# Optimization experiments

Hardware: AMD Instinct MI355X
Metric: run time of the kernel (lower is better)

Reference implementation:

```python
import jax, jax.numpy as jnp
import numpy as np

N, D = 16384, 512
LOGIT_SCALE = 14.285714  # 1/0.07, standard CLIP temperature


def setup_inputs() -> dict:
    key = jax.random.key(0)
    k1, k2 = jax.random.split(key)
    image_features = jax.random.normal(k1, (N, D), dtype=jnp.float32)
    text_features = jax.random.normal(k2, (N, D), dtype=jnp.float32)
    logit_scale = jnp.asarray(LOGIT_SCALE, dtype=jnp.float32)
    return {
        "image_features": image_features,
        "text_features": text_features,
        "logit_scale": logit_scale,
    }


def reference(image_features, text_features, logit_scale):
    # logits_per_image = scale * img @ txt.T  -> [N, N]
    # logits_per_text is its transpose, so compute the GEMM once.
    logits = logit_scale * jnp.einsum("nd,md->nm", image_features, text_features)
    diag = jnp.diagonal(logits)  # correct-pair logits (labels = arange)
    # cross_entropy with label i on row i: logsumexp(row) - logit[i,i]
    loss_i = jnp.mean(jax.nn.logsumexp(logits, axis=1) - diag)
    # text loss uses transposed logits -> column-wise logsumexp
    loss_t = jnp.mean(jax.nn.logsumexp(logits, axis=0) - diag)
    return (loss_i + loss_t) * 0.5
```

## Files before the change

### kernel.cpp

```cpp
#include <hip/hip_runtime.h>
#include <hip/hip_bf16.h>

#define N_ 16384
#define D_ 512
#define BM 256
#define BN 256
#define BK 64
#define NT (D_ / BK)
#define NBLK (N_ / BM)
#define BUFB 32768

typedef __attribute__((ext_vector_type(8))) __bf16 bf16x8;
typedef __attribute__((ext_vector_type(4))) float f32x4;

#define GLDS(gptr, lptr)                                                              \
  __builtin_amdgcn_global_load_lds((const __attribute__((address_space(1))) void*)(gptr), \
                                   (__attribute__((address_space(3))) void*)(lptr), 16, 0, 0)

__device__ inline unsigned short f2bf(float f) {
  __hip_bfloat16 h = __float2bfloat16(f);
  return *reinterpret_cast<unsigned short*>(&h);
}

__global__ void cvt_bf16_kernel(const float* __restrict__ src,
                                unsigned short* __restrict__ dst, long n,
                                const float* __restrict__ scale_p) {
  const float s = scale_p ? scale_p[0] : 1.0f;
  long i = ((long)blockIdx.x * blockDim.x + threadIdx.x) * 8;
  const long stride = (long)gridDim.x * blockDim.x * 8;
  typedef __attribute__((ext_vector_type(8))) unsigned short us8;
  for (; i < n; i += stride) {
    const float4* sp = (const float4*)(src + i);
    float4 f0 = sp[0], f1 = sp[1];
    us8 v;
    v[0] = f2bf(f0.x * s); v[1] = f2bf(f0.y * s); v[2] = f2bf(f0.z * s); v[3] = f2bf(f0.w * s);
    v[4] = f2bf(f1.x * s); v[5] = f2bf(f1.y * s); v[6] = f2bf(f1.z * s); v[7] = f2bf(f1.w * s);
    *(us8*)(dst + i) = v;
  }
}

__global__ __launch_bounds__(512, 2)
void gemm_lse_kernel(const unsigned short* __restrict__ A,
                     const unsigned short* __restrict__ B,
                     float2* __restrict__ rowMS,
                     float2* __restrict__ colMS,
                     float* __restrict__ diag) {
  __shared__ __align__(16) unsigned short As[2][BM][BK];
  __shared__ __align__(16) unsigned short Bs[2][BN][BK];

  const int t = threadIdx.x;
  const int l = t & 63;
  const int wid = t >> 6;
  const int wr = wid >> 2;
  const int wc = wid & 3;

  int id = blockIdx.x;
  id = (id & 7) * (NBLK * NBLK / 8) + (id >> 3);
  const int br = id / NBLK;
  const int bc = id % NBLK;

  const int srow = t >> 3;
  const int scol = (((t & 7) ^ (srow & 7)) << 3);

  const unsigned short* aBase = A + (size_t)(br * BM + srow) * D_ + scol;
  const unsigned short* bBase = B + (size_t)(bc * BN + srow) * D_ + scol;

  f32x4 acc[8][4];
#pragma unroll
  for (int m = 0; m < 8; ++m)
#pragma unroll
    for (int n = 0; n < 4; ++n) acc[m][n] = (f32x4)0.0f;

  const int swz = (l & 7) << 4;
  const char* asb = (const char*)As;
  const char* bsb = (const char*)Bs;

#define STAGE(kt_, b_)                                              \
  {                                                                 \
    const unsigned short* ag_ = aBase + (kt_)*BK;                   \
    const unsigned short* bg_ = bBase + (kt_)*BK;                   \
    char* al_ = (char*)As + (b_)*BUFB + t * 16;                     \
    char* bl_ = (char*)Bs + (b_)*BUFB + t * 16;                     \
    _Pragma("unroll") for (int c_ = 0; c_ < 4; ++c_) {              \
      GLDS(ag_ + c_ * 64 * D_, al_ + c_ * 8192);                    \
      GLDS(bg_ + c_ * 64 * D_, bl_ + c_ * 8192);                    \
    }                                                               \
  }

  STAGE(0, 0);
  STAGE(1, 1);

#pragma unroll
  for (int kt = 0; kt < NT; ++kt) {
    const int b = kt & 1;
    if (kt == NT - 1) { asm volatile("s_waitcnt vmcnt(0)" ::: "memory"); }
    else              { asm volatile("s_waitcnt vmcnt(8)" ::: "memory"); }
    __builtin_amdgcn_sched_barrier(0);
    __builtin_amdgcn_s_barrier();
    __builtin_amdgcn_sched_barrier(0);

#pragma unroll
    for (int kk = 0; kk < 2; ++kk) {
      const int cbk = kk * 64 + (l >> 4) * 16;
      bf16x8 af[8], bfv[4];
#pragma unroll
      for (int m = 0; m < 8; ++m)
        af[m] = *(const bf16x8*)(asb + b * BUFB +
                                 (wr * 128 + m * 16 + (l & 15)) * 128 + (cbk ^ swz));
#pragma unroll
      for (int n = 0; n < 4; ++n)
        bfv[n] = *(const bf16x8*)(bsb + b * BUFB +
                                  (wc * 64 + n * 16 + (l & 15)) * 128 + (cbk ^ swz));
      __builtin_amdgcn_s_setprio(1);
#pragma unroll
      for (int m = 0; m < 8; ++m)
#pragma unroll
        for (int n = 0; n < 4; ++n)
          acc[m][n] = __builtin_amdgcn_mfma_f32_16x16x32_bf16(af[m], bfv[n], acc[m][n], 0, 0, 0);
      __builtin_amdgcn_s_setprio(0);
    }

    asm volatile("s_waitcnt lgkmcnt(0)" ::: "memory");
    __builtin_amdgcn_sched_barrier(0);
    __builtin_amdgcn_s_barrier();
    __builtin_amdgcn_sched_barrier(0);
    if (kt + 2 < NT) STAGE(kt + 2, b);
  }
#undef STAGE

  float* rowb = (float*)As;
  float* colb = rowb + 4 * 256 * 2;

  if (br == bc) {
#pragma unroll
    for (int m = 0; m < 8; ++m)
#pragma unroll
      for (int n = 0; n < 4; ++n)
#pragma unroll
        for (int r = 0; r < 4; ++r) {
          const int row = wr * 128 + m * 16 + (l >> 4) * 4 + r;
          const int col = wc * 64 + n * 16 + (l & 15);
          if (row == col) diag[br * BM + row] = acc[m][n][r];
        }
  }

#pragma unroll
  for (int m = 0; m < 8; ++m) {
#pragma unroll
    for (int r = 0; r < 4; ++r) {
      float mx = fmaxf(fmaxf(acc[m][0][r], acc[m][1][r]), fmaxf(acc[m][2][r], acc[m][3][r]));
#pragma unroll
      for (int off = 1; off < 16; off <<= 1) mx = fmaxf(mx, __shfl_xor(mx, off, 64));
      float s = 0.f;
#pragma unroll
      for (int n = 0; n < 4; ++n) s += __expf(acc[m][n][r] - mx);
#pragma unroll
      for (int off = 1; off < 16; off <<= 1) s += __shfl_xor(s, off, 64);
      if ((l & 15) == 0) {
        const int row = wr * 128 + m * 16 + (l >> 4) * 4 + r;
        rowb[(wc * 256 + row) * 2 + 0] = mx;
        rowb[(wc * 256 + row) * 2 + 1] = s;
      }
    }
  }

#pragma unroll
  for (int n = 0; n < 4; ++n) {
    float mx = -1e30f;
#pragma unroll
    for (int m = 0; m < 8; ++m)
#pragma unroll
      for (int r = 0; r < 4; ++r) mx = fmaxf(mx, acc[m][n][r]);
    mx = fmaxf(mx, __shfl_xor(mx, 16, 64));
    mx = fmaxf(mx, __shfl_xor(mx, 32, 64));
    float s = 0.f;
#pragma unroll
    for (int m = 0; m < 8; ++m)
#pragma unroll
      for (int r = 0; r < 4; ++r) s += __expf(acc[m][n][r] - mx);
    s += __shfl_xor(s, 16, 64);
    s += __shfl_xor(s, 32, 64);
    if ((l >> 4) == 0) {
      const int col = wc * 64 + n * 16 + l;
      colb[(wr * 256 + col) * 2 + 0] = mx;
      colb[(wr * 256 + col) * 2 + 1] = s;
    }
  }
  __syncthreads();

  if (t < 256) {
    float mm = -1e30f, ss = 0.f;
#pragma unroll
    for (int w = 0; w < 4; ++w) {
      float m0 = rowb[(w * 256 + t) * 2 + 0], s0 = rowb[(w * 256 + t) * 2 + 1];
      float nm = fmaxf(mm, m0);
      ss = ss * __expf(mm - nm) + s0 * __expf(m0 - nm);
      mm = nm;
    }
    rowMS[(size_t)bc * N_ + br * BM + t] = make_float2(mm, ss);
  } else {
    const int c = t - 256;
    float mm = -1e30f, ss = 0.f;
#pragma unroll
    for (int w = 0; w < 2; ++w) {
      float m0 = colb[(w * 256 + c) * 2 + 0], s0 = colb[(w * 256 + c) * 2 + 1];
      float nm = fmaxf(mm, m0);
      ss = ss * __expf(mm - nm) + s0 * __expf(m0 - nm);
      mm = nm;
    }
    colMS[(size_t)br * N_ + bc * BN + c] = make_float2(mm, ss);
  }
}

__global__ void reduce1_kernel(const float2* __restrict__ rowMS,
                               const float2* __restrict__ colMS,
                               const float* __restrict__ diag,
                               float* __restrict__ partials) {
  const int tid = blockIdx.x * blockDim.x + threadIdx.x;
  float m = -1e30f, s = 0.f;
  if (tid < N_) {
    const int r = tid;
    for (int cb = 0; cb < NBLK; ++cb) {
      float2 p = rowMS[(size_t)cb * N_ + r];
      float nm = fmaxf(m, p.x);
      s = s * __expf(m - nm) + p.y * __expf(p.x - nm);
      m = nm;
    }
    m = m + logf(s) - diag[r];
  } else {
    const int c = tid - N_;
    for (int rb = 0; rb < NBLK; ++rb) {
      float2 p = colMS[(size_t)rb * N_ + c];
      float nm = fmaxf(m, p.x);
      s = s * __expf(m - nm) + p.y * __expf(p.x - nm);
      m = nm;
    }
    m = m + logf(s) - diag[c];
  }
  float val = m;
#pragma unroll
  for (int off = 1; off < 64; off <<= 1) val += __shfl_xor(val, off, 64);
  __shared__ float red[4];
  if ((threadIdx.x & 63) == 0) red[threadIdx.x >> 6] = val;
  __syncthreads();
  if (threadIdx.x == 0) partials[blockIdx.x] = red[0] + red[1] + red[2] + red[3];
}

__global__ void reduce2_kernel(const float* __restrict__ partials, float* __restrict__ out) {
  const int t = threadIdx.x;
  float v = partials[t] + partials[t + 64];
#pragma unroll
  for (int off = 1; off < 64; off <<= 1) v += __shfl_xor(v, off, 64);
  if (t == 0) out[0] = v * (1.0f / (2.0f * (float)N_));
}

extern "C" void kernel_launch(void* const* d_in, const int* in_sizes, int n_in,
                              void* d_out, int out_size, void* d_ws, size_t ws_size,
                              hipStream_t stream) {
  const float* img = (const float*)d_in[0];
  const float* txt = (const float*)d_in[1];
  const float* scale = (const float*)d_in[2];
  float* out = (float*)d_out;

  char* ws = (char*)d_ws;
  size_t off = 0;
  unsigned short* imgB = (unsigned short*)(ws + off); off += (size_t)N_ * D_ * 2;
  unsigned short* txtB = (unsigned short*)(ws + off); off += (size_t)N_ * D_ * 2;
  float2* rowMS = (float2*)(ws + off); off += (size_t)NBLK * N_ * sizeof(float2);
  float2* colMS = (float2*)(ws + off); off += (size_t)NBLK * N_ * sizeof(float2);
  float* diag = (float*)(ws + off); off += (size_t)N_ * sizeof(float);
  float* partials = (float*)(ws + off); off += 128 * sizeof(float);
  (void)ws_size; (void)in_sizes; (void)n_in; (void)out_size;

  cvt_bf16_kernel<<<1024, 256, 0, stream>>>(img, imgB, (long)N_ * D_, scale);
  cvt_bf16_kernel<<<1024, 256, 0, stream>>>(txt, txtB, (long)N_ * D_, nullptr);
  gemm_lse_kernel<<<NBLK * NBLK, 512, 0, stream>>>(imgB, txtB, rowMS, colMS, diag);
  reduce1_kernel<<<(2 * N_) / 256, 256, 0, stream>>>(rowMS, colMS, diag, partials);
  reduce2_kernel<<<1, 64, 0, stream>>>(partials, out);
}
```

Measured before the change: 468.7 us.

## Restructure GEMM main loop into fine-grained phases interleaving LDS loads, prefetch and MFMA

Splits each K tile into two 32-wide halves stored as separate LDS regions with a new rotation-based swizzle. The loop becomes four phases per tile, each loading fragments, issuing part of the next global-to-LDS prefetch, then running a block of MFMAs between barriers. This is meant to overlap global loads, LDS reads and matrix math more evenly and to reduce bank conflicts. It adds more barriers per tile and tighter vmcnt bookkeeping, which could introduce stalls or races if the wait counts are off.

Measured after the change: 511.9 us. +9.2%, slower.

```diff
diff --git a/kernel.cpp b/kernel.cpp
--- a/kernel.cpp
+++ b/kernel.cpp
@@ -8,7 +8,7 @@
 #define BK 64
 #define NT (D_ / BK)
 #define NBLK (N_ / BM)
-#define BUFB 32768
+#define REGB 16384
 
 typedef __attribute__((ext_vector_type(8))) __bf16 bf16x8;
 typedef __attribute__((ext_vector_type(4))) float f32x4;
@@ -16,6 +16,8 @@
 #define GLDS(gptr, lptr)                                                              \
   __builtin_amdgcn_global_load_lds((const __attribute__((address_space(1))) void*)(gptr), \
                                    (__attribute__((address_space(3))) void*)(lptr), 16, 0, 0)
+
+#define MFMA(a, b, c) __builtin_amdgcn_mfma_f32_16x16x32_bf16((a), (b), (c), 0, 0, 0)
 
 __device__ inline unsigned short f2bf(float f) {
   __hip_bfloat16 h = __float2bfloat16(f);
@@ -45,8 +47,8 @@
                      float2* __restrict__ rowMS,
                      float2* __restrict__ colMS,
                      float* __restrict__ diag) {
-  __shared__ __align__(16) unsigned short As[2][BM][BK];
-  __shared__ __align__(16) unsigned short Bs[2][BN][BK];
+  __shared__ __align__(16) unsigned short As[2][2][256][32];
+  __shared__ __align__(16) unsigned short Bs[2][2][256][32];
 
   const int t = threadIdx.x;
   const int l = t & 63;
@@ -59,11 +61,23 @@
   const int br = id / NBLK;
   const int bc = id % NBLK;
 
-  const int srow = t >> 3;
-  const int scol = (((t & 7) ^ (srow & 7)) << 3);
-
-  const unsigned short* aBase = A + (size_t)(br * BM + srow) * D_ + scol;
-  const unsigned short* bBase = B + (size_t)(bc * BN + srow) * D_ + scol;
+  const int sr0 = t >> 2;
+  const int sc0 = ((t & 3) - (t >> 3)) & 3;
+
+  const unsigned short* aSt = A + (size_t)(br * BM + sr0) * D_ + sc0 * 8;
+  const unsigned short* bSt = B + (size_t)(bc * BN + sr0) * D_ + sc0 * 8;
+
+  int offA[8], offB[4];
+#pragma unroll
+  for (int m = 0; m < 8; ++m) {
+    const int row = wr * 128 + m * 16 + (l & 15);
+    offA[m] = row * 64 + ((((l >> 4) + (row >> 1)) & 3) << 4);
+  }
+#pragma unroll
+  for (int n = 0; n < 4; ++n) {
+    const int row = wc * 64 + n * 16 + (l & 15);
+    offB[n] = row * 64 + ((((l >> 4) + (row >> 1)) & 3) << 4);
+  }
 
   f32x4 acc[8][4];
 #pragma unroll
@@ -71,62 +85,99 @@
 #pragma unroll
     for (int n = 0; n < 4; ++n) acc[m][n] = (f32x4)0.0f;
 
-  const int swz = (l & 7) << 4;
   const char* asb = (const char*)As;
   const char* bsb = (const char*)Bs;
-
-#define STAGE(kt_, b_)                                              \
-  {                                                                 \
-    const unsigned short* ag_ = aBase + (kt_)*BK;                   \
-    const unsigned short* bg_ = bBase + (kt_)*BK;                   \
-    char* al_ = (char*)As + (b_)*BUFB + t * 16;                     \
-    char* bl_ = (char*)Bs + (b_)*BUFB + t * 16;                     \
-    _Pragma("unroll") for (int c_ = 0; c_ < 4; ++c_) {              \
-      GLDS(ag_ + c_ * 64 * D_, al_ + c_ * 8192);                    \
-      GLDS(bg_ + c_ * 64 * D_, bl_ + c_ * 8192);                    \
-    }                                                               \
-  }
-
-  STAGE(0, 0);
-  STAGE(1, 1);
-
-#pragma unroll
-  for (int kt = 0; kt < NT; ++kt) {
-    const int b = kt & 1;
-    if (kt == NT - 1) { asm volatile("s_waitcnt vmcnt(0)" ::: "memory"); }
-    else              { asm volatile("s_waitcnt vmcnt(8)" ::: "memory"); }
-    __builtin_amdgcn_sched_barrier(0);
-    __builtin_amdgcn_s_barrier();
-    __builtin_amdgcn_sched_barrier(0);
-
-#pragma unroll
-    for (int kk = 0; kk < 2; ++kk) {
-      const int cbk = kk * 64 + (l >> 4) * 16;
-      bf16x8 af[8], bfv[4];
-#pragma unroll
-      for (int m = 0; m < 8; ++m)
-        af[m] = *(const bf16x8*)(asb + b * BUFB +
-                                 (wr * 128 + m * 16 + (l & 15)) * 128 + (cbk ^ swz));
-#pragma unroll
-      for (int n = 0; n < 4; ++n)
-        bfv[n] = *(const bf16x8*)(bsb + b * BUFB +
-                                  (wc * 64 + n * 16 + (l & 15)) * 128 + (cbk ^ swz));
-      __builtin_amdgcn_s_setprio(1);
-#pragma unroll
-      for (int m = 0; m < 8; ++m)
-#pragma unroll
-        for (int n = 0; n < 4; ++n)
-          acc[m][n] = __builtin_amdgcn_mfma_f32_16x16x32_bf16(af[m], bfv[n], acc[m][n], 0, 0, 0);
-      __builtin_amdgcn_s_setprio(0);
-    }
-
-    asm volatile("s_waitcnt lgkmcnt(0)" ::: "memory");
-    __builtin_amdgcn_sched_barrier(0);
-    __builtin_amdgcn_s_barrier();
-    __builtin_amdgcn_sched_barrier(0);
-    if (kt + 2 < NT) STAGE(kt + 2, b);
-  }
-#undef STAGE
+  bf16x8 af[8], bfv[4];
+
+#define STG(gbase, lds, S_, K_, kt_)                                   \
+  {                                                                    \
+    const unsigned short* g_ = (gbase) + (kt_)*BK + (K_)*32;           \
+    char* d_ = (char*)(lds) + ((S_)*2 + (K_)) * REGB + t * 16;         \
+    GLDS(g_, d_);                                                      \
+    GLDS(g_ + 128 * D_, d_ + 8192);                                    \
+  }
+
+  STG(aSt, As, 0, 0, 0); STG(bSt, Bs, 0, 0, 0);
+  STG(aSt, As, 0, 1, 0); STG(bSt, Bs, 0, 1, 0);
+  STG(aSt, As, 1, 0, 1); STG(bSt, Bs, 1, 0, 1);
+  STG(aSt, As, 1, 1, 1);
+  asm volatile("s_waitcnt vmcnt(6)" ::: "memory");
+  __builtin_amdgcn_sched_barrier(0);
+  __builtin_amdgcn_s_barrier();
+
+#define PH_SYNC()                                          \
+  __builtin_amdgcn_s_barrier();                            \
+  asm volatile("s_waitcnt lgkmcnt(0)" ::: "memory");       \
+  __builtin_amdgcn_sched_barrier(0);                       \
+  __builtin_amdgcn_s_setprio(1);
+
+#define PH_END()                                           \
+  __builtin_amdgcn_s_setprio(0);                           \
+  __builtin_amdgcn_s_barrier();
+
+#define TILE(T_, S_)                                                          \
+  {                                                                           \
+                                                   \
+    _Pragma("unroll") for (int m = 0; m < 8; ++m)                             \
+        af[m] = *(const bf16x8*)(asb + ((S_)*2 + 0) * REGB + offA[m]);        \
+    bfv[0] = *(const bf16x8*)(bsb + ((S_)*2 + 0) * REGB + offB[0]);           \
+    bfv[1] = *(const bf16x8*)(bsb + ((S_)*2 + 0) * REGB + offB[1]);           \
+    if ((T_) + 1 < NT) STG(bSt, Bs, ((S_) ^ 1), 1, (T_) + 1);                 \
+    if ((T_) == NT - 1) {                                                     \
+      asm volatile("s_waitcnt vmcnt(0)" ::: "memory");                        \
+      __builtin_amdgcn_sched_barrier(0);                                      \
+    }                                                                         \
+    PH_SYNC();                                                                \
+    _Pragma("unroll") for (int m = 0; m < 8; ++m) {                           \
+      acc[m][0] = MFMA(af[m], bfv[0], acc[m][0]);                             \
+      acc[m][1] = MFMA(af[m], bfv[1], acc[m][1]);                             \
+    }                                                                         \
+    PH_END();                                                                 \
+                                                   \
+    bfv[2] = *(const bf16x8*)(bsb + ((S_)*2 + 0) * REGB + offB[2]);           \
+    bfv[3] = *(const bf16x8*)(bsb + ((S_)*2 + 0) * REGB + offB[3]);           \
+    if ((T_) + 2 < NT) STG(aSt, As, (S_), 0, (T_) + 2);                       \
+    PH_SYNC();                                                                \
+    _Pragma("unroll") for (int m = 0; m < 8; ++m) {                           \
+      acc[m][2] = MFMA(af[m], bfv[2], acc[m][2]);                             \
+      acc[m][3] = MFMA(af[m], bfv[3], acc[m][3]);                             \
+    }                                                                         \
+    PH_END();                                                                 \
+                                                   \
+    _Pragma("unroll") for (int m = 0; m < 8; ++m)                             \
+        af[m] = *(const bf16x8*)(asb + ((S_)*2 + 1) * REGB + offA[m]);        \
+    bfv[0] = *(const bf16x8*)(bsb + ((S_)*2 + 1) * REGB + offB[0]);           \
+    bfv[1] = *(const bf16x8*)(bsb + ((S_)*2 + 1) * REGB + offB[1]);           \
+    if ((T_) + 2 < NT) STG(bSt, Bs, (S_), 0, (T_) + 2);                       \
+    PH_SYNC();                                                                \
+    _Pragma("unroll") for (int m = 0; m < 8; ++m) {                           \
+      acc[m][0] = MFMA(af[m], bfv[0], acc[m][0]);                             \
+      acc[m][1] = MFMA(af[m], bfv[1], acc[m][1]);                             \
+    }                                                                         \
+    PH_END();                                                                 \
+                                                   \
+    bfv[2] = *(const bf16x8*)(bsb + ((S_)*2 + 1) * REGB + offB[2]);           \
+    bfv[3] = *(const bf16x8*)(bsb + ((S_)*2 + 1) * REGB + offB[3]);           \
+    if ((T_) + 2 < NT) STG(aSt, As, (S_), 1, (T_) + 2);                       \
+    asm volatile("s_waitcnt vmcnt(6)" ::: "memory");                          \
+    __builtin_amdgcn_sched_barrier(0);                                        \
+    PH_SYNC();                                                                \
+    _Pragma("unroll") for (int m = 0; m < 8; ++m) {                           \
+      acc[m][2] = MFMA(af[m], bfv[2], acc[m][2]);                             \
+      acc[m][3] = MFMA(af[m], bfv[3], acc[m][3]);                             \
+    }                                                                         \
+    PH_END();                                                                 \
+  }
+
+#pragma unroll 1
+  for (int tp = 0; tp < NT; tp += 2) {
+    TILE(tp, 0);
+    TILE(tp + 1, 1);
+  }
+#undef TILE
+#undef PH_SYNC
+#undef PH_END
+#undef STG
 
   float* rowb = (float*)As;
   float* colb = rowb + 4 * 256 * 2;
```

## Triple-buffer BK=32 LDS pipeline with split A/B staging and exp2-domain softmax

Applied to the files above, without the earlier changes.

Reworks the GEMM main loop from a double-buffered BK=64 scheme to a three-slot BK=32 ring. Each k-step is split into two half-M MFMA phases, with A and B prefetches interleaved between them and finer vmcnt waits, so loads overlap compute more closely. It also changes the block-index swizzle and the LDS swizzle pattern, and keeps separate LDS arrays for the epilogue reductions. Separately, log2(e) is folded into the bf16 conversion scale so the epilogue can use exp2f and log2f, with ln2 applied back at the end. The extra barriers per k-step and the smaller K tile could add synchronization overhead.

Measured after the change: 501.1 us. 1.07x slower.

```diff
diff --git a/kernel.cpp b/kernel.cpp
--- a/kernel.cpp
+++ b/kernel.cpp
@@ -5,10 +5,10 @@
 #define D_ 512
 #define BM 256
 #define BN 256
-#define BK 64
+#define BK 32
 #define NT (D_ / BK)
 #define NBLK (N_ / BM)
-#define BUFB 32768
+#define SLOTB 16384
 
 typedef __attribute__((ext_vector_type(8))) __bf16 bf16x8;
 typedef __attribute__((ext_vector_type(4))) float f32x4;
@@ -17,6 +17,8 @@
   __builtin_amdgcn_global_load_lds((const __attribute__((address_space(1))) void*)(gptr), \
                                    (__attribute__((address_space(3))) void*)(lptr), 16, 0, 0)
 
+#define MFMA16(a, b, c) __builtin_amdgcn_mfma_f32_16x16x32_bf16((a), (b), (c), 0, 0, 0)
+
 __device__ inline unsigned short f2bf(float f) {
   __hip_bfloat16 h = __float2bfloat16(f);
   return *reinterpret_cast<unsigned short*>(&h);
@@ -25,7 +27,7 @@
 __global__ void cvt_bf16_kernel(const float* __restrict__ src,
                                 unsigned short* __restrict__ dst, long n,
                                 const float* __restrict__ scale_p) {
-  const float s = scale_p ? scale_p[0] : 1.0f;
+  const float s = scale_p ? scale_p[0] * 1.4426950408889634f : 1.0f;
   long i = ((long)blockIdx.x * blockDim.x + threadIdx.x) * 8;
   const long stride = (long)gridDim.x * blockDim.x * 8;
   typedef __attribute__((ext_vector_type(8))) unsigned short us8;
@@ -45,8 +47,10 @@
                      float2* __restrict__ rowMS,
                      float2* __restrict__ colMS,
                      float* __restrict__ diag) {
-  __shared__ __align__(16) unsigned short As[2][BM][BK];
-  __shared__ __align__(16) unsigned short Bs[2][BN][BK];
+  __shared__ __align__(16) unsigned short AL[3][2][128][32];
+  __shared__ __align__(16) unsigned short BL[3][2][128][32];
+  __shared__ float rowb[4][256][2];
+  __shared__ float colb[2][256][2];
 
   const int t = threadIdx.x;
   const int l = t & 63;
@@ -54,16 +58,32 @@
   const int wr = wid >> 2;
   const int wc = wid & 3;
 
-  int id = blockIdx.x;
-  id = (id & 7) * (NBLK * NBLK / 8) + (id >> 3);
-  const int br = id / NBLK;
-  const int bc = id % NBLK;
-
-  const int srow = t >> 3;
-  const int scol = (((t & 7) ^ (srow & 7)) << 3);
-
-  const unsigned short* aBase = A + (size_t)(br * BM + srow) * D_ + scol;
-  const unsigned short* bBase = B + (size_t)(bc * BN + srow) * D_ + scol;
+  const int id = blockIdx.x;
+  const int w = id >> 3;
+  const int bc = (id & 7) * 8 + (w & 7);
+  const int br = w >> 3;
+
+  const int srow = t >> 2;
+  const int scol = ((t & 3) ^ ((t >> 3) & 3)) * 8;
+
+  const unsigned short* aS = A + (size_t)(br * BM + srow) * D_ + scol;
+  const unsigned short* bS = B + (size_t)(bc * BN + srow) * D_ + scol;
+
+  int offA[2][4], offB[4];
+#pragma unroll
+  for (int qm = 0; qm < 2; ++qm)
+#pragma unroll
+    for (int m = 0; m < 4; ++m) {
+      const int rowh = qm * 64 + m * 16 + (l & 15);
+      offA[qm][m] = wr * 8192 + rowh * 64 + ((((l >> 4) ^ (rowh >> 1)) & 3) << 4);
+    }
+#pragma unroll
+  for (int n = 0; n < 4; ++n) {
+    const int colh = (wc & 1) * 64 + n * 16 + (l & 15);
+    offB[n] = (wc >> 1) * 8192 + colh * 64 + ((((l >> 4) ^ (colh >> 1)) & 3) << 4);
+  }
+  const char* asb = (const char*)AL;
+  const char* bsb = (const char*)BL;
 
   f32x4 acc[8][4];
 #pragma unroll
@@ -71,65 +91,68 @@
 #pragma unroll
     for (int n = 0; n < 4; ++n) acc[m][n] = (f32x4)0.0f;
 
-  const int swz = (l & 7) << 4;
-  const char* asb = (const char*)As;
-  const char* bsb = (const char*)Bs;
-
-#define STAGE(kt_, b_)                                              \
-  {                                                                 \
-    const unsigned short* ag_ = aBase + (kt_)*BK;                   \
-    const unsigned short* bg_ = bBase + (kt_)*BK;                   \
-    char* al_ = (char*)As + (b_)*BUFB + t * 16;                     \
-    char* bl_ = (char*)Bs + (b_)*BUFB + t * 16;                     \
-    _Pragma("unroll") for (int c_ = 0; c_ < 4; ++c_) {              \
-      GLDS(ag_ + c_ * 64 * D_, al_ + c_ * 8192);                    \
-      GLDS(bg_ + c_ * 64 * D_, bl_ + c_ * 8192);                    \
-    }                                                               \
-  }
-
-  STAGE(0, 0);
-  STAGE(1, 1);
-
-#pragma unroll
-  for (int kt = 0; kt < NT; ++kt) {
-    const int b = kt & 1;
-    if (kt == NT - 1) { asm volatile("s_waitcnt vmcnt(0)" ::: "memory"); }
-    else              { asm volatile("s_waitcnt vmcnt(8)" ::: "memory"); }
-    __builtin_amdgcn_sched_barrier(0);
+#define STG_A(kt_, S_)                                                      \
+  {                                                                         \
+    GLDS(aS + (kt_)*BK, (char*)AL + (S_)*SLOTB + t * 16);                   \
+    GLDS(aS + 128 * D_ + (kt_)*BK, (char*)AL + (S_)*SLOTB + 8192 + t * 16); \
+  }
+#define STG_B(kt_, S_)                                                      \
+  {                                                                         \
+    GLDS(bS + (kt_)*BK, (char*)BL + (S_)*SLOTB + t * 16);                   \
+    GLDS(bS + 128 * D_ + (kt_)*BK, (char*)BL + (S_)*SLOTB + 8192 + t * 16); \
+  }
+
+  STG_A(0, 0); STG_B(0, 0);
+  STG_A(1, 1); STG_B(1, 1);
+  asm volatile("s_waitcnt vmcnt(4)" ::: "memory");
+  __builtin_amdgcn_sched_barrier(0);
+  __builtin_amdgcn_s_barrier();
+
+#pragma unroll
+  for (int T = 0; T < NT; ++T) {
+    const int S = T % 3;
+    const int SP = (T + 2) % 3;
+    bf16x8 af[4], bf[4];
+
+#pragma unroll
+    for (int m = 0; m < 4; ++m) af[m] = *(const bf16x8*)(asb + S * SLOTB + offA[0][m]);
+#pragma unroll
+    for (int n = 0; n < 4; ++n) bf[n] = *(const bf16x8*)(bsb + S * SLOTB + offB[n]);
+    if (T + 2 < NT) STG_A(T + 2, SP);
     __builtin_amdgcn_s_barrier();
-    __builtin_amdgcn_sched_barrier(0);
-
-#pragma unroll
-    for (int kk = 0; kk < 2; ++kk) {
-      const int cbk = kk * 64 + (l >> 4) * 16;
-      bf16x8 af[8], bfv[4];
-#pragma unroll
-      for (int m = 0; m < 8; ++m)
-        af[m] = *(const bf16x8*)(asb + b * BUFB +
-                                 (wr * 128 + m * 16 + (l & 15)) * 128 + (cbk ^ swz));
-#pragma unroll
-      for (int n = 0; n < 4; ++n)
-        bfv[n] = *(const bf16x8*)(bsb + b * BUFB +
-                                  (wc * 64 + n * 16 + (l & 15)) * 128 + (cbk ^ swz));
-      __builtin_amdgcn_s_setprio(1);
-#pragma unroll
-      for (int m = 0; m < 8; ++m)
-#pragma unroll
-        for (int n = 0; n < 4; ++n)
-          acc[m][n] = __builtin_amdgcn_mfma_f32_16x16x32_bf16(af[m], bfv[n], acc[m][n], 0, 0, 0);
-      __builtin_amdgcn_s_setprio(0);
-    }
-
     asm volatile("s_waitcnt lgkmcnt(0)" ::: "memory");
     __builtin_amdgcn_sched_barrier(0);
+    __builtin_amdgcn_s_setprio(1);
+#pragma unroll
+    for (int m = 0; m < 4; ++m)
+#pragma unroll
+      for (int n = 0; n < 4; ++n) acc[m][n] = MFMA16(af[m], bf[n], acc[m][n]);
+    __builtin_amdgcn_s_setprio(0);
     __builtin_amdgcn_s_barrier();
+
+#pragma unroll
+    for (int m = 0; m < 4; ++m) af[m] = *(const bf16x8*)(asb + S * SLOTB + offA[1][m]);
+    if (T + 2 < NT) STG_B(T + 2, SP);
+    if (T <= NT - 3) {
+      asm volatile("s_waitcnt vmcnt(4)" ::: "memory");
+      __builtin_amdgcn_sched_barrier(0);
+    } else if (T == NT - 2) {
+      asm volatile("s_waitcnt vmcnt(0)" ::: "memory");
+      __builtin_amdgcn_sched_barrier(0);
+    }
+    __builtin_amdgcn_s_barrier();
+    asm volatile("s_waitcnt lgkmcnt(0)" ::: "memory");
     __builtin_amdgcn_sched_barrier(0);
-    if (kt + 2 < NT) STAGE(kt + 2, b);
-  }
-#undef STAGE
-
-  float* rowb = (float*)As;
-  float* colb = rowb + 4 * 256 * 2;
+    __builtin_amdgcn_s_setprio(1);
+#pragma unroll
+    for (int m = 0; m < 4; ++m)
+#pragma unroll
+      for (int n = 0; n < 4; ++n) acc[4 + m][n] = MFMA16(af[m], bf[n], acc[4 + m][n]);
+    __builtin_amdgcn_s_setprio(0);
+    __builtin_amdgcn_s_barrier();
+  }
+#undef STG_A
+#undef STG_B
 
   if (br == bc) {
 #pragma unroll
@@ -153,13 +176,13 @@
       for (int off = 1; off < 16; off <<= 1) mx = fmaxf(mx, __shfl_xor(mx, off, 64));
       float s = 0.f;
 #pragma unroll
-      for (int n = 0; n < 4; ++n) s += __expf(acc[m][n][r] - mx);
+      for (int n = 0; n < 4; ++n) s += exp2f(acc[m][n][r] - mx);
 #pragma unroll
       for (int off = 1; off < 16; off <<= 1) s += __shfl_xor(s, off, 64);
       if ((l & 15) == 0) {
         const int row = wr * 128 + m * 16 + (l >> 4) * 4 + r;
-        rowb[(wc * 256 + row) * 2 + 0] = mx;
-        rowb[(wc * 256 + row) * 2 + 1] = s;
+        rowb[wc][row][0] = mx;
+        rowb[wc][row][1] = s;
       }
     }
   }
@@ -177,13 +200,13 @@
 #pragma unroll
     for (int m = 0; m < 8; ++m)
 #pragma unroll
-      for (int r = 0; r < 4; ++r) s += __expf(acc[m][n][r] - mx);
+      for (int r = 0; r < 4; ++r) s += exp2f(acc[m][n][r] - mx);
     s += __shfl_xor(s, 16, 64);
     s += __shfl_xor(s, 32, 64);
     if ((l >> 4) == 0) {
       const int col = wc * 64 + n * 16 + l;
-      colb[(wr * 256 + col) * 2 + 0] = mx;
-      colb[(wr * 256 + col) * 2 + 1] = s;
+      colb[wr][col][0] = mx;
+      colb[wr][col][1] = s;
     }
   }
   __syncthreads();
@@ -191,10 +214,10 @@
   if (t < 256) {
     float mm = -1e30f, ss = 0.f;
 #pragma unroll
-    for (int w = 0; w < 4; ++w) {
-      float m0 = rowb[(w * 256 + t) * 2 + 0], s0 = rowb[(w * 256 + t) * 2 + 1];
+    for (int wv = 0; wv < 4; ++wv) {
+      float m0 = rowb[wv][t][0], s0 = rowb[wv][t][1];
       float nm = fmaxf(mm, m0);
-      ss = ss * __expf(mm - nm) + s0 * __expf(m0 - nm);
+      ss = ss * exp2f(mm - nm) + s0 * exp2f(m0 - nm);
       mm = nm;
     }
     rowMS[(size_t)bc * N_ + br * BM + t] = make_float2(mm, ss);
@@ -202,10 +225,10 @@
     const int c = t - 256;
     float mm = -1e30f, ss = 0.f;
 #pragma unroll
-    for (int w = 0; w < 2; ++w) {
-      float m0 = colb[(w * 256 + c) * 2 + 0], s0 = colb[(w * 256 + c) * 2 + 1];
+    for (int wv = 0; wv < 2; ++wv) {
+      float m0 = colb[wv][c][0], s0 = colb[wv][c][1];
       float nm = fmaxf(mm, m0);
-      ss = ss * __expf(mm - nm) + s0 * __expf(m0 - nm);
+      ss = ss * exp2f(mm - nm) + s0 * exp2f(m0 - nm);
       mm = nm;
     }
     colMS[(size_t)br * N_ + bc * BN + c] = make_float2(mm, ss);
@@ -223,19 +246,19 @@
     for (int cb = 0; cb < NBLK; ++cb) {
       float2 p = rowMS[(size_t)cb * N_ + r];
       float nm = fmaxf(m, p.x);
-      s = s * __expf(m - nm) + p.y * __expf(p.x - nm);
+      s = s * exp2f(m - nm) + p.y * exp2f(p.x - nm);
       m = nm;
     }
-    m = m + logf(s) - diag[r];
+    m = m + log2f(s) - diag[r];
   } else {
     const int c = tid - N_;
     for (int rb = 0; rb < NBLK; ++rb) {
       float2 p = colMS[(size_t)rb * N_ + c];
       float nm = fmaxf(m, p.x);
-      s = s * __expf(m - nm) + p.y * __expf(p.x - nm);
+      s = s * exp2f(m - nm) + p.y * exp2f(p.x - nm);
       m = nm;
     }
-    m = m + logf(s) - diag[c];
+    m = m + log2f(s) - diag[c];
   }
   float val = m;
 #pragma unroll
@@ -251,7 +274,7 @@
   float v = partials[t] + partials[t + 64];
 #pragma unroll
   for (int off = 1; off < 64; off <<= 1) v += __shfl_xor(v, off, 64);
-  if (t == 0) out[0] = v * (1.0f / (2.0f * (float)N_));
+  if (t == 0) out[0] = v * (0.69314718055994531f / (2.0f * (float)N_));
 }
 
 extern "C" void kernel_launch(void* const* d_in, const int* in_sizes, int n_in,
```
